# Performance work log

Hardware: AMD Instinct MI355X
Metric: run time of the kernel (lower is better)

The kernel has to match this reference:

```python
import jax, jax.numpy as jnp
import numpy as np

B, S, D = 2, 2048, 1024
H, DA, DL = 8, 64, 64   # heads, attention_dim, linear_dim
L = 2                    # num_blocks


def _layernorm(x, w, b, eps):
    mu = jnp.mean(x, axis=-1, keepdims=True)
    var = jnp.mean(jnp.square(x - mu), axis=-1, keepdims=True)
    return (x - mu) * jax.lax.rsqrt(var + eps) * w + b


def _norm_no_affine(x, eps):
    mu = jnp.mean(x, axis=-1, keepdims=True)
    var = jnp.mean(jnp.square(x - mu), axis=-1, keepdims=True)
    return (x - mu) * jax.lax.rsqrt(var + eps)


def setup_inputs() -> dict:
    key = jax.random.key(0)
    ks = jax.random.split(key, 8)
    x = jax.random.normal(ks[0], (B, S, D), dtype=jnp.float32)
    # causal visibility mask: True = visible
    attn_mask = jnp.tril(jnp.ones((S, S), dtype=bool))[None].repeat(B, axis=0)
    proj_dim = DL * 2 * H + DA * 2 * H  # 2048
    uvqk = jax.random.normal(ks[1], (L, D, proj_dim), dtype=jnp.float32) * 0.02
    o_w = jax.random.normal(ks[2], (L, D, DL * H), dtype=jnp.float32) * 0.02  # torch [out,in]
    o_b = jnp.zeros((L, D), dtype=jnp.float32)
    ln_w = jnp.ones((L, D), dtype=jnp.float32)
    ln_b = jnp.zeros((L, D), dtype=jnp.float32)
    last_ln_w = jnp.ones((D,), dtype=jnp.float32)
    last_ln_b = jnp.zeros((D,), dtype=jnp.float32)
    return {"x": x, "attn_mask": attn_mask, "uvqk": uvqk, "o_w": o_w,
            "o_b": o_b, "ln_w": ln_w, "ln_b": ln_b,
            "last_ln_w": last_ln_w, "last_ln_b": last_ln_b}


def reference(x, attn_mask, uvqk, o_w, o_b, ln_w, ln_b, last_ln_w, last_ln_b):
    seq_len = x.shape[1]
    m = attn_mask[:, None, :, :]  # [B,1,S,S]
    for i in range(L):
        h = _layernorm(x, ln_w[i], ln_b[i], 1e-6)                 # [B,S,D]
        proj = jax.nn.silu(jnp.einsum('bsd,de->bse', h, uvqk[i]))  # [B,S,2*(DL+DA)*H]
        u, v, q, k = jnp.split(proj, [DL * H, 2 * DL * H, 2 * DL * H + DA * H], axis=-1)
        q = q.reshape(B, seq_len, H, DA).transpose(0, 2, 1, 3)   # [B,H,S,DA]
        kk = k.reshape(B, seq_len, H, DA).transpose(0, 2, 1, 3)
        vv = v.reshape(B, seq_len, H, DL).transpose(0, 2, 1, 3)  # [B,H,S,DL]
        uu = u.reshape(B, seq_len, H, DL).transpose(0, 2, 1, 3)
        scores = jnp.einsum('bhsd,bhtd->bhst', q, kk)            # [B,H,S,S]
        scores = jnp.where(m, jax.nn.silu(scores) / seq_len, 0.0)
        out = jnp.einsum('bhst,bhtd->bhsd', scores, vv)          # [B,H,S,DL]
        out = _norm_no_affine(out, 1e-6)
        u_dot = (uu * out).transpose(0, 2, 1, 3).reshape(B, seq_len, DL * H)
        x = x + jnp.einsum('bsf,df->bsd', u_dot, o_w[i]) + o_b[i]
    return _layernorm(x, last_ln_w, last_ln_b, 1e-8)
```

## Files before the change

### kernel.cpp

```cpp
#include <hip/hip_runtime.h>

#define B_ 2
#define S_ 2048
#define D_ 1024
#define H_ 8
#define L_ 2
#define P_ 2048
#define F_ 512
#define R_ (B_*S_)

typedef unsigned short u16;
typedef unsigned int u32;
typedef __bf16 bf16;
typedef bf16 bf16x8 __attribute__((ext_vector_type(8)));
typedef short short8 __attribute__((ext_vector_type(8)));
typedef float v4f __attribute__((ext_vector_type(4)));

__device__ __forceinline__ float silu_fast(float x){
  float e = __expf(-x);
  return x * __builtin_amdgcn_rcpf(1.0f + e);
}
__device__ __forceinline__ float bf2f(u16 u){
  union { u32 i; float f; } x; x.i = ((u32)u) << 16; return x.f;
}
__device__ __forceinline__ u16 f2bfu(float f){
  union { float f; u32 i; } x; x.f = f;
  u32 r = x.i + 0x7fff + ((x.i >> 16) & 1);
  return (u16)(r >> 16);
}
__device__ __forceinline__ void gload16(const u16* g, u16* l){
  __builtin_amdgcn_global_load_lds(
      (const __attribute__((address_space(1))) void*)g,
      (__attribute__((address_space(3))) void*)l, 16, 0, 0);
}

__global__ __launch_bounds__(256) void cvt_bf16_kernel(const float* __restrict__ src, u16* __restrict__ dst){
  int i = (blockIdx.x * 256 + threadIdx.x) * 4;
  float4 v = *(const float4*)(src + i);
  ushort4 o; o.x = f2bfu(v.x); o.y = f2bfu(v.y); o.z = f2bfu(v.z); o.w = f2bfu(v.w);
  *(ushort4*)(dst + i) = o;
}

__global__ __launch_bounds__(256) void cvt_uvqkT_kernel(const float* __restrict__ uvqk, u16* __restrict__ ot){
  __shared__ float t[32][33];
  int l = blockIdx.z;
  int p0 = blockIdx.x * 32, d0 = blockIdx.y * 32;
  int tx = threadIdx.x & 31, ty = threadIdx.x >> 5;
  const float* src = uvqk + ((size_t)l * D_ + d0) * P_ + p0;
  #pragma unroll
  for (int s = 0; s < 4; s++)
    t[ty + s*8][tx] = src[(size_t)(ty + s*8) * P_ + tx];
  __syncthreads();
  u16* dst = ot + ((size_t)l * P_ + p0) * D_ + d0;
  #pragma unroll
  for (int s = 0; s < 4; s++)
    dst[(size_t)(ty + s*8) * D_ + tx] = f2bfu(t[tx][ty + s*8]);
}

__global__ __launch_bounds__(256) void kvpack_kernel(const u16* __restrict__ projh,
    u16* __restrict__ kpack, u16* __restrict__ vpack){
  __shared__ u16 tls[64*72];
  int t = blockIdx.x, t0 = t * 64;
  int bh = blockIdx.y;
  int b = bh >> 3, hh = bh & 7;
  int tid = threadIdx.x;
  const size_t bS = (size_t)b * S_;
  const int voff = F_ + hh*64, koff = 3*F_ + hh*64;
  {
    int row = tid >> 2, c16 = (tid & 3) * 16;
    const u16* sp = projh + (bS + t0 + row) * P_ + voff + c16;
    short8 a = *(const short8*)sp;
    short8 bq = *(const short8*)(sp + 8);
    *(short8*)&tls[row*72 + c16] = a;
    *(short8*)&tls[row*72 + c16 + 8] = bq;
  }
  __syncthreads();
  size_t obase = ((size_t)(bh*32 + t) * 8) * 512;
  #pragma unroll
  for (int pass = 0; pass < 2; pass++){
    int id = tid + pass * 256;
    int c = id >> 6, lane = id & 63;
    int quad = lane >> 4, l15 = lane & 15;
    int cns = c >> 1, ckst = c & 1;
    const u16* kp = projh + (bS + t0 + cns*16 + l15) * P_ + koff + ckst*32 + quad*8;
    *(short8*)(kpack + obase + (size_t)c*512 + lane*8) = *(const short8*)kp;
    short8 vv;
    #pragma unroll
    for (int j = 0; j < 8; j++)
      vv[j] = (short)tls[(ckst*32 + quad*8 + j)*72 + cns*16 + l15];
    *(short8*)(vpack + obase + (size_t)c*512 + lane*8) = vv;
  }
}

__global__ __launch_bounds__(256) void ln_kernel(const float* __restrict__ src,
    const float* __restrict__ w, const float* __restrict__ b,
    void* __restrict__ outp, float eps, int out_bf16){
  int row = blockIdx.x, tid = threadIdx.x;
  const float* xr = src + (size_t)row * D_;
  float4 v = *(const float4*)(xr + tid * 4);
  float s  = v.x + v.y + v.z + v.w;
  float sq = v.x*v.x + v.y*v.y + v.z*v.z + v.w*v.w;
  #pragma unroll
  for (int off = 32; off; off >>= 1){ s += __shfl_down(s, off); sq += __shfl_down(sq, off); }
  __shared__ float red[8];
  __shared__ float stats[2];
  int wid = tid >> 6;
  if ((tid & 63) == 0){ red[wid] = s; red[4 + wid] = sq; }
  __syncthreads();
  if (tid == 0){
    float S1 = red[0] + red[1] + red[2] + red[3];
    float S2 = red[4] + red[5] + red[6] + red[7];
    float mu = S1 * (1.0f / D_);
    float var = S2 * (1.0f / D_) - mu * mu;
    stats[0] = mu; stats[1] = rsqrtf(var + eps);
  }
  __syncthreads();
  float mu = stats[0], rs = stats[1];
  int i = tid * 4;
  float4 wv = *(const float4*)(w + i);
  float4 bv = *(const float4*)(b + i);
  float o0 = (v.x - mu) * rs * wv.x + bv.x;
  float o1 = (v.y - mu) * rs * wv.y + bv.y;
  float o2 = (v.z - mu) * rs * wv.z + bv.z;
  float o3 = (v.w - mu) * rs * wv.w + bv.w;
  if (out_bf16){
    ushort4 o; o.x = f2bfu(o0); o.y = f2bfu(o1); o.z = f2bfu(o2); o.w = f2bfu(o3);
    *(ushort4*)((u16*)outp + (size_t)row * D_ + i) = o;
  } else {
    *(float4*)((float*)outp + (size_t)row * D_ + i) = make_float4(o0, o1, o2, o3);
  }
}

template<int KDIM>
__device__ __forceinline__ void gemm_mfma_core(const u16* __restrict__ A,
    const u16* __restrict__ Bt, u16* As, u16* Bs, int m0, int n0, v4f acc[4][4]){
  int tid = threadIdx.x;
  int w = tid >> 6, lane = tid & 63;
  int wm = w >> 1, wn = w & 1, quad = lane >> 4, l15 = lane & 15;
  int srow = lane >> 2, skoct = (lane & 3) * 8;
  for (int kt = 0; kt < KDIM; kt += 32){
    __syncthreads();
    #pragma unroll
    for (int s = 0; s < 2; s++){
      int g = w * 2 + s;
      gload16(A  + (size_t)(m0 + g*16 + srow) * KDIM + kt + skoct, As + g*512);
      gload16(Bt + (size_t)(n0 + g*16 + srow) * KDIM + kt + skoct, Bs + g*512);
    }
    __syncthreads();
    short8 af[4], bfr[4];
    #pragma unroll
    for (int i = 0; i < 4; i++)
      af[i] = *(const short8*)&As[(wm*64 + i*16 + l15)*32 + quad*8];
    #pragma unroll
    for (int j = 0; j < 4; j++)
      bfr[j] = *(const short8*)&Bs[(wn*64 + j*16 + l15)*32 + quad*8];
    #pragma unroll
    for (int i = 0; i < 4; i++)
      #pragma unroll
      for (int j = 0; j < 4; j++)
        acc[i][j] = __builtin_amdgcn_mfma_f32_16x16x32_bf16(
            __builtin_bit_cast(bf16x8, af[i]), __builtin_bit_cast(bf16x8, bfr[j]),
            acc[i][j], 0, 0, 0);
  }
}

__global__ __launch_bounds__(256) void gemm_silu_mfma(const u16* __restrict__ A,
    const u16* __restrict__ Bt, u16* __restrict__ C){
  __shared__ u16 As[128*32], Bs[128*32];
  v4f acc[4][4];
  #pragma unroll
  for (int i = 0; i < 4; i++)
    #pragma unroll
    for (int j = 0; j < 4; j++) acc[i][j] = (v4f){0.f,0.f,0.f,0.f};
  int f = blockIdx.x;
  int wg = (f & 7) * 64 + (f >> 3);
  int bx = wg & 15, by = wg >> 4;
  int m0 = by * 128, n0 = bx * 128;
  gemm_mfma_core<D_>(A, Bt, As, Bs, m0, n0, acc);
  int tid = threadIdx.x, w = tid >> 6, lane = tid & 63;
  int wm = w >> 1, wn = w & 1, quad = lane >> 4, l15 = lane & 15;
  #pragma unroll
  for (int i = 0; i < 4; i++)
    #pragma unroll
    for (int r = 0; r < 4; r++){
      int m = m0 + wm*64 + i*16 + quad*4 + r;
      u16* cp = C + (size_t)m * P_ + n0 + wn*64 + l15;
      #pragma unroll
      for (int j = 0; j < 4; j++)
        cp[j*16] = f2bfu(silu_fast(acc[i][j][r]));
    }
}

__global__ __launch_bounds__(256) void gemm_add_mfma(const u16* __restrict__ A,
    const u16* __restrict__ Bt, const float* __restrict__ bias,
    const float* __restrict__ Xin, float* __restrict__ Xout){
  __shared__ u16 As[128*32], Bs[128*32];
  v4f acc[4][4];
  #pragma unroll
  for (int i = 0; i < 4; i++)
    #pragma unroll
    for (int j = 0; j < 4; j++) acc[i][j] = (v4f){0.f,0.f,0.f,0.f};
  int f = blockIdx.x;
  int wg = (f & 7) * 32 + (f >> 3);
  int bx = wg & 7, by = wg >> 3;
  int m0 = by * 128, n0 = bx * 128;
  gemm_mfma_core<F_>(A, Bt, As, Bs, m0, n0, acc);
  int tid = threadIdx.x, w = tid >> 6, lane = tid & 63;
  int wm = w >> 1, wn = w & 1, quad = lane >> 4, l15 = lane & 15;
  float bj[4];
  #pragma unroll
  for (int j = 0; j < 4; j++) bj[j] = bias[n0 + wn*64 + j*16 + l15];
  #pragma unroll
  for (int i = 0; i < 4; i++)
    #pragma unroll
    for (int r = 0; r < 4; r++){
      int m = m0 + wm*64 + i*16 + quad*4 + r;
      size_t off = (size_t)m * D_ + n0 + wn*64 + l15;
      const float* xi = Xin + off;
      float* xo = Xout + off;
      #pragma unroll
      for (int j = 0; j < 4; j++)
        xo[j*16] = xi[j*16] + acc[i][j][r] + bj[j];
    }
}

__global__ __launch_bounds__(256) void attn_kernel(const u16* __restrict__ projh,
                                                   const u16* __restrict__ kpack,
                                                   const u16* __restrict__ vpack,
                                                   u16* __restrict__ opart){
  __shared__ u16 ks[8*512];
  __shared__ u16 vs[8*512];
  __shared__ u16 Ps[64*72];
  int f = (int)blockIdx.x;
  int g = f & 7;
  int s = f >> 3;
  int c = s & 31;
  int slot = s >> 5;
  int z = c >> 4;
  int x = c & 15;
  int qt = slot ? x : (15 - x);
  int bh = g + (slot << 3);
  int ttop = 2*qt + 1;
  int b = bh >> 3, hh = bh & 7;
  int tid = threadIdx.x;
  int w = tid >> 6, lane = tid & 63, quad = lane >> 4, l15 = lane & 15;
  int s0 = qt * 128;
  const size_t bS = (size_t)b * S_;
  const int qoff = 2*F_ + hh*64;

  bf16x8 aq[2][2];
  #pragma unroll
  for (int qh = 0; qh < 2; qh++){
    const u16* qp = projh + (bS + s0 + qh*64 + w*16 + l15) * P_ + qoff + quad*8;
    aq[qh][0] = __builtin_bit_cast(bf16x8, *(const short8*)qp);
    aq[qh][1] = __builtin_bit_cast(bf16x8, *(const short8*)(qp + 32));
  }

  v4f oacc[2][4];
  #pragma unroll
  for (int qh = 0; qh < 2; qh++)
    #pragma unroll
    for (int i = 0; i < 4; i++) oacc[qh][i] = (v4f){0.f, 0.f, 0.f, 0.f};

  for (int t = z; t <= ttop; t += 2){
    size_t pbase = ((size_t)(bh*32 + t) * 8) * 512;
    __syncthreads();
    #pragma unroll
    for (int cc = 0; cc < 2; cc++){
      int ch = w + cc*4;
      gload16(kpack + pbase + (size_t)ch*512 + lane*8, ks + ch*512);
      gload16(vpack + pbase + (size_t)ch*512 + lane*8, vs + ch*512);
    }
    __syncthreads();

    short8 vf[4][2];
    #pragma unroll
    for (int ds = 0; ds < 4; ds++)
      #pragma unroll
      for (int kst = 0; kst < 2; kst++)
        vf[ds][kst] = *(const short8*)&vs[(ds*2+kst)*512 + lane*8];

    #pragma unroll
    for (int qh = 0; qh < 2; qh++){
      int dtile = 2*qt + qh;
      if (t > dtile) continue;
      v4f sacc[4];
      #pragma unroll
      for (int i = 0; i < 4; i++) sacc[i] = (v4f){0.f, 0.f, 0.f, 0.f};
      #pragma unroll
      for (int ns = 0; ns < 4; ns++){
        bf16x8 bk0 = __builtin_bit_cast(bf16x8, *(const short8*)&ks[(ns*2+0)*512 + lane*8]);
        bf16x8 bk1 = __builtin_bit_cast(bf16x8, *(const short8*)&ks[(ns*2+1)*512 + lane*8]);
        sacc[ns] = __builtin_amdgcn_mfma_f32_16x16x32_bf16(aq[qh][0], bk0, sacc[ns], 0, 0, 0);
        sacc[ns] = __builtin_amdgcn_mfma_f32_16x16x32_bf16(aq[qh][1], bk1, sacc[ns], 0, 0, 0);
      }

      bool diag = (t == dtile);
      #pragma unroll
      for (int ns = 0; ns < 4; ns++){
        #pragma unroll
        for (int r = 0; r < 4; r++){
          int rl = w*16 + quad*4 + r;
          int cl = ns*16 + l15;
          float p = silu_fast(sacc[ns][r]) * (1.0f / S_);
          if (diag && cl > rl) p = 0.0f;
          Ps[rl*72 + cl] = f2bfu(p);
        }
      }
      #pragma unroll
      for (int kst = 0; kst < 2; kst++){
        short8 aps = *(const short8*)&Ps[(w*16 + l15)*72 + kst*32 + quad*8];
        bf16x8 ap = __builtin_bit_cast(bf16x8, aps);
        #pragma unroll
        for (int ds = 0; ds < 4; ds++)
          oacc[qh][ds] = __builtin_amdgcn_mfma_f32_16x16x32_bf16(
              ap, __builtin_bit_cast(bf16x8, vf[ds][kst]), oacc[qh][ds], 0, 0, 0);
      }
    }
  }

  u16* ob = opart + (size_t)z * ((size_t)R_ * F_);
  #pragma unroll
  for (int qh = 0; qh < 2; qh++){
    #pragma unroll
    for (int r = 0; r < 4; r++){
      int sg = s0 + qh*64 + w*16 + quad*4 + r;
      u16* op = ob + (bS + sg) * (size_t)F_ + hh*64 + l15;
      #pragma unroll
      for (int ds = 0; ds < 4; ds++)
        op[ds*16] = f2bfu(oacc[qh][ds][r]);
    }
  }
}

__global__ __launch_bounds__(256) void norm_gate_kernel(const u16* __restrict__ opart,
    const u16* __restrict__ projh, u16* __restrict__ udot){
  int w = threadIdx.x >> 6, lane = threadIdx.x & 63;
  int sg = blockIdx.x * 4 + w;
  int hh = lane >> 3, seg = lane & 7;
  size_t off = (size_t)sg * F_ + hh*64 + seg*8;
  short8 a0 = *(const short8*)(opart + off);
  short8 a1 = *(const short8*)(opart + (size_t)R_ * F_ + off);
  float e[8];
  float s = 0.f, sq = 0.f;
  #pragma unroll
  for (int i = 0; i < 8; i++){
    e[i] = bf2f((u16)a0[i]) + bf2f((u16)a1[i]);
    s += e[i]; sq += e[i]*e[i];
  }
  #pragma unroll
  for (int m = 1; m < 8; m <<= 1){
    s  += __shfl_xor(s, m, 64);
    sq += __shfl_xor(sq, m, 64);
  }
  float mu = s * (1.0f/64.0f);
  float var = sq * (1.0f/64.0f) - mu*mu;
  float rs = rsqrtf(var + 1e-6f);
  const u16* up = projh + (size_t)sg * P_ + hh*64 + seg*8;
  short8 uv = *(const short8*)up;
  short8 ov;
  #pragma unroll
  for (int i = 0; i < 8; i++)
    ov[i] = (short)f2bfu((e[i] - mu) * rs * bf2f((u16)uv[i]));
  *(short8*)(udot + off) = ov;
}

extern "C" void kernel_launch(void* const* d_in, const int* in_sizes, int n_in,
                              void* d_out, int out_size, void* d_ws, size_t ws_size,
                              hipStream_t stream){
  (void)in_sizes; (void)n_in; (void)out_size; (void)ws_size;
  const float* x     = (const float*)d_in[0];
  const float* uvqk  = (const float*)d_in[2];
  const float* o_w   = (const float*)d_in[3];
  const float* o_b   = (const float*)d_in[4];
  const float* ln_w  = (const float*)d_in[5];
  const float* ln_b  = (const float*)d_in[6];
  const float* lln_w = (const float*)d_in[7];
  const float* lln_b = (const float*)d_in[8];
  float* out = (float*)d_out;

  char* ws = (char*)d_ws;
  float* xf    = (float*)ws;
  u16*   h     = (u16*)(ws + (16u<<20));
  u16*   kpack = h;
  u16*   vpack = (u16*)(ws + (20u<<20));
  u16*   udot  = (u16*)(ws + (24u<<20));
  u16*   projh = (u16*)(ws + (28u<<20));
  u16*   uvqkT = (u16*)(ws + (44u<<20));
  u16*   owh   = (u16*)(ws + (52u<<20));
  u16*   opart = (u16*)(ws + (54u<<20));

  cvt_uvqkT_kernel<<<dim3(P_/32, D_/32, L_), 256, 0, stream>>>(uvqk, uvqkT);
  cvt_bf16_kernel<<<L_ * D_ * F_ / 1024, 256, 0, stream>>>(o_w, owh);
  for (int l = 0; l < L_; l++){
    const float* xsrc = (l == 0) ? x : xf;
    ln_kernel<<<R_, 256, 0, stream>>>(xsrc, ln_w + l * D_, ln_b + l * D_, h, 1e-6f, 1);
    gemm_silu_mfma<<<512, 256, 0, stream>>>(
        h, uvqkT + (size_t)l * P_ * D_, projh);
    kvpack_kernel<<<dim3(S_/64, B_*H_), 256, 0, stream>>>(projh, kpack, vpack);
    attn_kernel<<<512, 256, 0, stream>>>(projh, kpack, vpack, opart);
    norm_gate_kernel<<<R_/4, 256, 0, stream>>>(opart, projh, udot);
    gemm_add_mfma<<<256, 256, 0, stream>>>(
        udot, owh + (size_t)l * D_ * F_, o_b + l * D_, xsrc, xf);
  }
  ln_kernel<<<R_, 256, 0, stream>>>(xf, lln_w, lln_b, out, 1e-8f, 0);
}
```

Before: 297.1 us.

## Load K/V fragments directly to registers with double-buffered prefetch in attention

Drops the LDS staging of the K and V tiles, and with it the two block-wide barriers per iteration. Each lane now reads its pre-packed K/V fragments straight from global memory into registers. Two register sets alternate so the next tile's loads are issued before the current tile's MFMA work, overlapping memory latency with compute. This raises register pressure (64 extra VGPRs for the second set), which may cut occupancy. Each wave also now fetches the full K/V tile itself instead of the block sharing one copy through LDS.

Measured after the change: 280.1 us. 5.7% less time.

```diff
diff --git a/kernel.cpp b/kernel.cpp
--- a/kernel.cpp
+++ b/kernel.cpp
@@ -228,8 +228,6 @@
                                                    const u16* __restrict__ kpack,
                                                    const u16* __restrict__ vpack,
                                                    u16* __restrict__ opart){
-  __shared__ u16 ks[8*512];
-  __shared__ u16 vs[8*512];
   __shared__ u16 Ps[64*72];
   int f = (int)blockIdx.x;
   int g = f & 7;
@@ -262,24 +260,16 @@
     #pragma unroll
     for (int i = 0; i < 4; i++) oacc[qh][i] = (v4f){0.f, 0.f, 0.f, 0.f};
 
-  for (int t = z; t <= ttop; t += 2){
-    size_t pbase = ((size_t)(bh*32 + t) * 8) * 512;
-    __syncthreads();
-    #pragma unroll
-    for (int cc = 0; cc < 2; cc++){
-      int ch = w + cc*4;
-      gload16(kpack + pbase + (size_t)ch*512 + lane*8, ks + ch*512);
-      gload16(vpack + pbase + (size_t)ch*512 + lane*8, vs + ch*512);
-    }
-    __syncthreads();
-
-    short8 vf[4][2];
-    #pragma unroll
-    for (int ds = 0; ds < 4; ds++)
-      #pragma unroll
-      for (int kst = 0; kst < 2; kst++)
-        vf[ds][kst] = *(const short8*)&vs[(ds*2+kst)*512 + lane*8];
-
+  auto LOADT = [&](short8 (&BK)[4][2], short8 (&VF)[4][2], int tt){
+    size_t pb = ((size_t)(bh*32 + tt) * 8) * 512;
+    #pragma unroll
+    for (int cc = 0; cc < 8; cc++){
+      BK[cc>>1][cc&1] = *(const short8*)(kpack + pb + (size_t)cc*512 + lane*8);
+      VF[cc>>1][cc&1] = *(const short8*)(vpack + pb + (size_t)cc*512 + lane*8);
+    }
+  };
+
+  auto COMPUTE = [&](const short8 (&BK)[4][2], const short8 (&VF)[4][2], int t){
     #pragma unroll
     for (int qh = 0; qh < 2; qh++){
       int dtile = 2*qt + qh;
@@ -289,12 +279,11 @@
       for (int i = 0; i < 4; i++) sacc[i] = (v4f){0.f, 0.f, 0.f, 0.f};
       #pragma unroll
       for (int ns = 0; ns < 4; ns++){
-        bf16x8 bk0 = __builtin_bit_cast(bf16x8, *(const short8*)&ks[(ns*2+0)*512 + lane*8]);
-        bf16x8 bk1 = __builtin_bit_cast(bf16x8, *(const short8*)&ks[(ns*2+1)*512 + lane*8]);
-        sacc[ns] = __builtin_amdgcn_mfma_f32_16x16x32_bf16(aq[qh][0], bk0, sacc[ns], 0, 0, 0);
-        sacc[ns] = __builtin_amdgcn_mfma_f32_16x16x32_bf16(aq[qh][1], bk1, sacc[ns], 0, 0, 0);
+        sacc[ns] = __builtin_amdgcn_mfma_f32_16x16x32_bf16(aq[qh][0],
+            __builtin_bit_cast(bf16x8, BK[ns][0]), sacc[ns], 0, 0, 0);
+        sacc[ns] = __builtin_amdgcn_mfma_f32_16x16x32_bf16(aq[qh][1],
+            __builtin_bit_cast(bf16x8, BK[ns][1]), sacc[ns], 0, 0, 0);
       }
-
       bool diag = (t == dtile);
       #pragma unroll
       for (int ns = 0; ns < 4; ns++){
@@ -314,8 +303,30 @@
         #pragma unroll
         for (int ds = 0; ds < 4; ds++)
           oacc[qh][ds] = __builtin_amdgcn_mfma_f32_16x16x32_bf16(
-              ap, __builtin_bit_cast(bf16x8, vf[ds][kst]), oacc[qh][ds], 0, 0, 0);
+              ap, __builtin_bit_cast(bf16x8, VF[ds][kst]), oacc[qh][ds], 0, 0, 0);
       }
+    }
+  };
+
+  short8 kA[4][2], vA[4][2], kB[4][2], vB[4][2];
+  int t = z;
+  LOADT(kA, vA, t);
+  for (;;){
+    if (t + 2 <= ttop){
+      LOADT(kB, vB, t + 2);
+      COMPUTE(kA, vA, t);
+      t += 2;
+    } else {
+      COMPUTE(kA, vA, t);
+      break;
+    }
+    if (t + 2 <= ttop){
+      LOADT(kA, vA, t + 2);
+      COMPUTE(kB, vB, t);
+      t += 2;
+    } else {
+      COMPUTE(kB, vB, t);
+      break;
     }
   }
 
```
